# Performance work log

Hardware: AMD Instinct MI355X
Metric: run time of the kernel (lower is better)

The kernel has to match this reference:

```python
import jax, jax.numpy as jnp
from jax import lax
import numpy as np

B, T, F_IN = 64, 3072, 128
CONV_OUT, K, STRIDE = 64, 3, 3
HID, OUT = 256, 10


def setup_inputs() -> dict:
    key = jax.random.key(0)
    ks = jax.random.split(key, 10)
    s = 0.05
    return {
        "input": jax.random.normal(ks[0], (B, T, F_IN), jnp.float32),
        "r": jnp.zeros(((T - K) // STRIDE + 1, B, CONV_OUT), jnp.float32),
        "hx0": jax.random.normal(ks[1], (B, HID), jnp.float32),
        "cx0": jax.random.normal(ks[2], (B, HID), jnp.float32),
        "conv_w": jax.random.normal(ks[3], (CONV_OUT, F_IN, K), jnp.float32) * s,
        "conv_b": jnp.zeros((CONV_OUT,), jnp.float32),
        "w_ih": jax.random.normal(ks[4], (4 * HID, CONV_OUT), jnp.float32) * s,
        "b_ih": jnp.zeros((4 * HID,), jnp.float32),
        "w_hh": jax.random.normal(ks[5], (4 * HID, HID), jnp.float32) * s,
        "b_hh": jnp.zeros((4 * HID,), jnp.float32),
        "lin_w": jax.random.normal(ks[6], (OUT, HID), jnp.float32) * s,
        "lin_b": jnp.zeros((OUT,), jnp.float32),
        "batch_size": B,
    }


def reference(input, r, hx0, cx0, conv_w, conv_b, w_ih, b_ih, w_hh, b_hh, lin_w, lin_b, batch_size):
    # F.normalize: L2 normalize along dim=1 (the time dim), eps=1e-12
    norm = jnp.sqrt(jnp.sum(input * input, axis=1, keepdims=True))
    x = input / jnp.maximum(norm, 1e-12)
    x = jnp.transpose(x, (0, 2, 1))  # [B, F_IN, T]
    x = lax.conv_general_dilated(
        x, conv_w, window_strides=(STRIDE,), padding='VALID',
        dimension_numbers=('NCH', 'OIH', 'NCH')) + conv_b[None, :, None]
    x = jax.nn.relu(x)
    x = jnp.transpose(x, (2, 0, 1))  # [T', B, 64]

    def step(carry, xt):
        h, c = carry
        gates = xt @ w_ih.T + b_ih + h @ w_hh.T + b_hh  # [B, 4H]
        i, f, g, o = jnp.split(gates, 4, axis=-1)
        c = jax.nn.sigmoid(f) * c + jax.nn.sigmoid(i) * jnp.tanh(g)
        h = jax.nn.sigmoid(o) * jnp.tanh(c)
        return (h, c), None

    (h, _), _ = lax.scan(step, (hx0, cx0), x)
    return h @ lin_w.T + lin_b  # [B, OUT]
```

## Files before the change

kernel.cpp:

```cpp
#include <hip/hip_runtime.h>
#include <math.h>

#define B_N 64
#define T_N 3072
#define FIN 128
#define TP 1024
#define COUT 64
#define HID 256
#define G4 1024
#define OUT_N 10
#define NCHUNK 24
#define CHUNK_T (T_N / NCHUNK)

#define WREG 24
#define WLDS 8

typedef _Float16 h2_t __attribute__((ext_vector_type(2)));
typedef unsigned u32x4 __attribute__((ext_vector_type(4)));

#if defined(__has_builtin)
#if __has_builtin(__builtin_amdgcn_fdot2)
#define HAVE_FDOT2 1
#endif
#endif

__device__ __forceinline__ float fdot2(unsigned w, unsigned h, float acc) {
#ifdef HAVE_FDOT2
    return __builtin_amdgcn_fdot2(__builtin_bit_cast(h2_t, w),
                                  __builtin_bit_cast(h2_t, h), acc, false);
#else
    h2_t wv = __builtin_bit_cast(h2_t, w), hv = __builtin_bit_cast(h2_t, h);
    return acc + (float)wv.x * (float)hv.x + (float)wv.y * (float)hv.y;
#endif
}

__device__ __forceinline__ unsigned pack2(float a, float b) {
    unsigned la = (unsigned)__builtin_bit_cast(unsigned short, (_Float16)a);
    unsigned lb = (unsigned)__builtin_bit_cast(unsigned short, (_Float16)b);
    return la | (lb << 16);
}

__global__ void pack_weights(const float* __restrict__ w_ih,
                             const float* __restrict__ w_hh,
                             unsigned* __restrict__ whhR,
                             unsigned* __restrict__ whhL,
                             float* __restrict__ wihT) {
    int col = blockIdx.x, d = threadIdx.x;
    const float* wr = w_hh + col * HID;
    unsigned p = pack2(wr[2 * d], wr[2 * d + 1]);
    int c = d >> 2, r = d & 3;
    if (c < WREG) whhR[(c * 1024 + col) * 4 + r] = p;
    else          whhL[((c - WREG) * 1024 + col) * 4 + r] = p;
    if (d < COUT) wihT[d * 1024 + col] = w_ih[col * COUT + d];
}

__global__ void prep_conv_w(const float* __restrict__ conv_w, float* __restrict__ wc2) {
    int i = blockIdx.x * 256 + threadIdx.x;
    if (i < 24576) {
        int j = i >> 6, oc = i & 63;
        int kk = j >> 7, ic = j & 127;
        wc2[i] = conv_w[(oc * 128 + ic) * 3 + kk];
    }
}

__global__ void norm_partial(const float* __restrict__ in, float* __restrict__ part) {
    int b = blockIdx.x, ch = blockIdx.y, f = threadIdx.x;
    const float* p = in + ((size_t)b * T_N + (size_t)ch * CHUNK_T) * FIN + f;
    float s0 = 0.f, s1 = 0.f, s2 = 0.f, s3 = 0.f;
#pragma unroll
    for (int r = 0; r < CHUNK_T; r += 4) {
        float v0 = p[(r + 0) * FIN];
        float v1 = p[(r + 1) * FIN];
        float v2 = p[(r + 2) * FIN];
        float v3 = p[(r + 3) * FIN];
        s0 += v0 * v0; s1 += v1 * v1; s2 += v2 * v2; s3 += v3 * v3;
    }
    part[(b * NCHUNK + ch) * FIN + f] = (s0 + s1) + (s2 + s3);
}

__global__ __launch_bounds__(256) void conv_relu(
        const float* __restrict__ in, const float* __restrict__ part,
        const float* __restrict__ wc2, const float* __restrict__ cb,
        float* __restrict__ X) {
    __shared__ __align__(16) float xs[16 * 384];
    __shared__ __align__(16) float wsh[96 * 64];
    __shared__ float invn[FIN];

    int b = blockIdx.x, tile = blockIdx.y;
    int tid = threadIdx.x;

    if (tid < FIN) {
        float s = 0.f;
#pragma unroll
        for (int c = 0; c < NCHUNK; c++) s += part[(b * NCHUNK + c) * FIN + tid];
        invn[tid] = rsqrtf(fmaxf(s, 1e-24f));
    }
    __syncthreads();

    const float* ip = in + ((size_t)b * T_N + (size_t)tile * 48) * FIN;
    for (int i = tid; i < 6144; i += 256) xs[i] = ip[i] * invn[i & 127];

    int oc = tid & 63, tq = tid >> 6;
    float acc0 = 0.f, acc1 = 0.f, acc2 = 0.f, acc3 = 0.f;
    const float* xb = xs + tq * 4 * 384;

    for (int c = 0; c < 4; c++) {
        __syncthreads();
        for (int i = tid; i < 6144; i += 256) wsh[i] = wc2[c * 6144 + i];
        __syncthreads();
#pragma unroll 8
        for (int jj = 0; jj < 96; jj += 4) {
            int j = c * 96 + jj;
            float w0 = wsh[(jj + 0) * 64 + oc];
            float w1 = wsh[(jj + 1) * 64 + oc];
            float w2 = wsh[(jj + 2) * 64 + oc];
            float w3 = wsh[(jj + 3) * 64 + oc];
            float4 x0 = *(const float4*)(xb + j);
            float4 x1 = *(const float4*)(xb + 384 + j);
            float4 x2 = *(const float4*)(xb + 768 + j);
            float4 x3 = *(const float4*)(xb + 1152 + j);
            acc0 += w0 * x0.x + w1 * x0.y + w2 * x0.z + w3 * x0.w;
            acc1 += w0 * x1.x + w1 * x1.y + w2 * x1.z + w3 * x1.w;
            acc2 += w0 * x2.x + w1 * x2.y + w2 * x2.z + w3 * x2.w;
            acc3 += w0 * x3.x + w1 * x3.y + w2 * x3.z + w3 * x3.w;
        }
    }
    float bb = cb[oc];
    int tp0 = tile * 16 + tq * 4;
    size_t o = ((size_t)b * TP + tp0) * COUT + oc;
    X[o]       = fmaxf(acc0 + bb, 0.f);
    X[o + 64]  = fmaxf(acc1 + bb, 0.f);
    X[o + 128] = fmaxf(acc2 + bb, 0.f);
    X[o + 192] = fmaxf(acc3 + bb, 0.f);
}

__global__ __launch_bounds__(256) void x_gemm(
        const float* __restrict__ X, const float* __restrict__ wihT,
        const float* __restrict__ b_ih, const float* __restrict__ b_hh,
        _Float16* __restrict__ xg) {
    __shared__ float xs[64 * 17];
    int b = blockIdx.x, t0 = blockIdx.y * 16, tid = threadIdx.x;

    const float* Xp = X + ((size_t)b * TP + t0) * COUT;
    for (int i = tid; i < 1024; i += 256) {
        int r = i >> 6, k = i & 63;
        xs[k * 17 + r] = Xp[i];
    }
    __syncthreads();

#pragma unroll
    for (int jt = 0; jt < 4; jt++) {
        int jj = jt * 256 + tid;
        float bias = b_ih[jj] + b_hh[jj];
        float acc[16];
#pragma unroll
        for (int r = 0; r < 16; r++) acc[r] = bias;
        for (int k = 0; k < 64; k++) {
            float w = wihT[k * 1024 + jj];
#pragma unroll
            for (int r = 0; r < 16; r++) acc[r] += w * xs[k * 17 + r];
        }
#pragma unroll
        for (int r = 0; r < 16; r++)
            xg[((size_t)b * TP + t0 + r) * 1024 + jj] = (_Float16)acc[r];
    }
}

__device__ __forceinline__ float fsig(float x) {
    return 1.f / (1.f + __expf(-x));
}
__device__ __forceinline__ float ftanh(float x) {
    float xc = fminf(fmaxf(x, -15.f), 15.f);
    float e = __expf(2.f * xc);
    return (e - 1.f) / (e + 1.f);
}

#define SM_WL   0
#define SM_H    131072
#define SM_FO   131584
#define SM_H32  133632
#define SM_SIZE 134656

#define REP24(M) M(0) M(1) M(2) M(3) M(4) M(5) M(6) M(7) M(8) M(9) M(10) M(11) \
                 M(12) M(13) M(14) M(15) M(16) M(17) M(18) M(19) M(20) M(21) M(22) M(23)
#define REP8(M)  M(0) M(1) M(2) M(3) M(4) M(5) M(6) M(7)

#define DECLW(n)  u32x4 wa##n, wb##n;
#define LOADW(n)  wa##n = whhR4[(n) * 1024 + j]; wb##n = whhR4[(n) * 1024 + j + 512];
#define DOTCH(n)  { u32x4 H = hs4[n]; \
    a0 = fdot2(wa##n[0], H[0], a0); a1 = fdot2(wb##n[0], H[0], a1); \
    a0 = fdot2(wa##n[1], H[1], a0); a1 = fdot2(wb##n[1], H[1], a1); \
    a0 = fdot2(wa##n[2], H[2], a0); a1 = fdot2(wb##n[2], H[2], a1); \
    a0 = fdot2(wa##n[3], H[3], a0); a1 = fdot2(wb##n[3], H[3], a1); }
#define DOTLDS(m) { u32x4 WA = wL[(m) * 1024 + j]; u32x4 WB = wL[(m) * 1024 + j + 512]; \
    u32x4 H = hs4[WREG + (m)]; \
    a0 = fdot2(WA[0], H[0], a0); a1 = fdot2(WB[0], H[0], a1); \
    a0 = fdot2(WA[1], H[1], a0); a1 = fdot2(WB[1], H[1], a1); \
    a0 = fdot2(WA[2], H[2], a0); a1 = fdot2(WB[2], H[2], a1); \
    a0 = fdot2(WA[3], H[3], a0); a1 = fdot2(WB[3], H[3], a1); }

__global__ __attribute__((amdgpu_flat_work_group_size(512, 512),
                          amdgpu_waves_per_eu(2, 2)))
void lstm_kernel(
        const u32x4* __restrict__ whhR4, const u32x4* __restrict__ whhL4,
        const _Float16* __restrict__ xg,
        const float* __restrict__ hx0, const float* __restrict__ cx0,
        const float* __restrict__ lin_w, const float* __restrict__ lin_b,
        float* __restrict__ out) {
    extern __shared__ char smem[];
    u32x4*    wL    = (u32x4*)(smem + SM_WL);
    _Float16* h_s   = (_Float16*)(smem + SM_H);
    float2*   fo_s  = (float2*)(smem + SM_FO);
    float*    h32_s = (float*)(smem + SM_H32);

    const int b = blockIdx.x, j = threadIdx.x;

    REP24(DECLW)
    REP24(LOADW)

    for (int i = j; i < WLDS * 1024; i += 512) wL[i] = whhL4[i];

    float c_reg = 0.f;
    if (j < HID) {
        c_reg = cx0[b * HID + j];
        h_s[j] = (_Float16)hx0[b * HID + j];
    }
    const _Float16* Xg = xg + (size_t)b * TP * G4;
    _Float16 xa = Xg[j], xb = Xg[j + 512];
    __syncthreads();

    const u32x4* hs4 = (const u32x4*)h_s;

    for (int t = 0; t < TP; t++) {
        _Float16 xan = (_Float16)0.f, xbn = (_Float16)0.f;
        if (t + 1 < TP) {
            xan = Xg[(t + 1) * G4 + j];
            xbn = Xg[(t + 1) * G4 + j + 512];
        }

        float a0 = (float)xa, a1 = (float)xb;
        REP24(DOTCH)
        REP8(DOTLDS)

        float s0 = 0.f, s1 = 0.f;
        if (j >= HID) {
            fo_s[j - HID] = make_float2(fsig(a0), fsig(a1));
        } else {
            s0 = fsig(a0);
            s1 = ftanh(a1);
        }
        __syncthreads();
        if (j < HID) {
            float2 fo = fo_s[j];
            c_reg = fo.x * c_reg + s0 * s1;
            float hh = fo.y * ftanh(c_reg);
            h_s[j] = (_Float16)hh;
            if (t == TP - 1) h32_s[j] = hh;
        }
        __syncthreads();
        xa = xan; xb = xbn;
    }

    if (j < OUT_N) {
        float s = lin_b[j];
        const float* lw = lin_w + j * HID;
#pragma unroll 4
        for (int k = 0; k < HID; k++) s += h32_s[k] * lw[k];
        out[b * OUT_N + j] = s;
    }
}

extern "C" void kernel_launch(void* const* d_in, const int* in_sizes, int n_in,
                              void* d_out, int out_size, void* d_ws, size_t ws_size,
                              hipStream_t stream) {
    const float* input  = (const float*)d_in[0];
    const float* hx0    = (const float*)d_in[2];
    const float* cx0    = (const float*)d_in[3];
    const float* conv_w = (const float*)d_in[4];
    const float* conv_b = (const float*)d_in[5];
    const float* w_ih   = (const float*)d_in[6];
    const float* b_ih   = (const float*)d_in[7];
    const float* w_hh   = (const float*)d_in[8];
    const float* b_hh   = (const float*)d_in[9];
    const float* lin_w  = (const float*)d_in[10];
    const float* lin_b  = (const float*)d_in[11];

    float* ws = (float*)d_ws;
    float*     part = ws;
    float*     X    = part + 196608;
    float*     wc2  = X + 4194304;
    float*     wihT = wc2 + 24576;
    unsigned*  whhR = (unsigned*)(wihT + 65536);
    unsigned*  whhL = whhR + WREG * 1024 * 4;
    _Float16*  xg   = (_Float16*)(whhL + WLDS * 1024 * 4);

    (void)hipFuncSetAttribute((const void*)lstm_kernel,
                              hipFuncAttributeMaxDynamicSharedMemorySize, SM_SIZE);

    pack_weights<<<1024, 128, 0, stream>>>(w_ih, w_hh, whhR, whhL, wihT);
    prep_conv_w<<<96, 256, 0, stream>>>(conv_w, wc2);
    norm_partial<<<dim3(B_N, NCHUNK), FIN, 0, stream>>>(input, part);
    conv_relu<<<dim3(B_N, 64), 256, 0, stream>>>(input, part, wc2, conv_b, X);
    x_gemm<<<dim3(B_N, 64), 256, 0, stream>>>(X, wihT, b_ih, b_hh, xg);
    lstm_kernel<<<B_N, 512, SM_SIZE, stream>>>(
        (const u32x4*)whhR, (const u32x4*)whhL, xg,
        hx0, cx0, lin_w, lin_b, (float*)d_out);
}
```

Before: 2.539 ms.

## Interleave LSTM gate columns to drop one barrier per step and broadcast h via readlane

Gate columns are permuted so each thread pair holds (i,g) and (f,o) for the same hidden unit. The cell update is then finished inside the pair with a DPP lane swap, which removes the fo_s LDS exchange and one __syncthreads per timestep. h is double-buffered in LDS, loaded once per wave as a uint2 per lane and broadcast with readlane instead of vector LDS reads. x_gemm now writes the matching interleaved fp16 pairs. The readlane calls add SALU work, and the column interleave must stay consistent across both packing kernels.

```diff
diff --git a/kernel.cpp b/kernel.cpp
--- a/kernel.cpp
+++ b/kernel.cpp
@@ -40,17 +40,39 @@
     return la | (lb << 16);
 }
 
+__device__ __forceinline__ int gperm(int c) {
+    int sub = (c >> 9) & 1;
+    int cc  = c & 511;
+    int slot = (cc < 256) ? (cc << 1) : (((cc - 256) << 1) | 1);
+    return slot | (sub << 9);
+}
+
+__device__ __forceinline__ float swap1(float x) {
+    int i = __builtin_bit_cast(int, x);
+#if defined(__has_builtin)
+#if __has_builtin(__builtin_amdgcn_mov_dpp)
+    int r = __builtin_amdgcn_mov_dpp(i, 0xB1, 0xF, 0xF, true);
+#else
+    int r = __shfl_xor(i, 1, 64);
+#endif
+#else
+    int r = __shfl_xor(i, 1, 64);
+#endif
+    return __builtin_bit_cast(float, r);
+}
+
 __global__ void pack_weights(const float* __restrict__ w_ih,
                              const float* __restrict__ w_hh,
                              unsigned* __restrict__ whhR,
                              unsigned* __restrict__ whhL,
                              float* __restrict__ wihT) {
     int col = blockIdx.x, d = threadIdx.x;
+    int pcol = gperm(col);
     const float* wr = w_hh + col * HID;
     unsigned p = pack2(wr[2 * d], wr[2 * d + 1]);
     int c = d >> 2, r = d & 3;
-    if (c < WREG) whhR[(c * 1024 + col) * 4 + r] = p;
-    else          whhL[((c - WREG) * 1024 + col) * 4 + r] = p;
+    if (c < WREG) whhR[(c * 1024 + pcol) * 4 + r] = p;
+    else          whhL[((c - WREG) * 1024 + pcol) * 4 + r] = p;
     if (d < COUT) wihT[d * 1024 + col] = w_ih[col * COUT + d];
 }
 
@@ -148,21 +170,30 @@
     }
     __syncthreads();
 
-#pragma unroll
-    for (int jt = 0; jt < 4; jt++) {
-        int jj = jt * 256 + tid;
-        float bias = b_ih[jj] + b_hh[jj];
-        float acc[16];
-#pragma unroll
-        for (int r = 0; r < 16; r++) acc[r] = bias;
+    unsigned* xgu = (unsigned*)xg;
+#pragma unroll
+    for (int half = 0; half < 2; half++) {
+        int cA = half * 512 + tid;
+        int cB = cA + 256;
+        float bA = b_ih[cA] + b_hh[cA];
+        float bB = b_ih[cB] + b_hh[cB];
+        float accA[16], accB[16];
+#pragma unroll
+        for (int r = 0; r < 16; r++) { accA[r] = bA; accB[r] = bB; }
         for (int k = 0; k < 64; k++) {
-            float w = wihT[k * 1024 + jj];
-#pragma unroll
-            for (int r = 0; r < 16; r++) acc[r] += w * xs[k * 17 + r];
+            float wA = wihT[k * 1024 + cA];
+            float wB = wihT[k * 1024 + cB];
+#pragma unroll
+            for (int r = 0; r < 16; r++) {
+                float xv = xs[k * 17 + r];
+                accA[r] += wA * xv;
+                accB[r] += wB * xv;
+            }
         }
 #pragma unroll
         for (int r = 0; r < 16; r++)
-            xg[((size_t)b * TP + t0 + r) * 1024 + jj] = (_Float16)acc[r];
+            xgu[((size_t)b * TP + t0 + r) * 512 + half * 256 + tid] =
+                pack2(accA[r], accB[r]);
     }
 }
 
@@ -177,9 +208,8 @@
 
 #define SM_WL   0
 #define SM_H    131072
-#define SM_FO   131584
-#define SM_H32  133632
-#define SM_SIZE 134656
+#define SM_H32  132096
+#define SM_SIZE 133120
 
 #define REP24(M) M(0) M(1) M(2) M(3) M(4) M(5) M(6) M(7) M(8) M(9) M(10) M(11) \
                  M(12) M(13) M(14) M(15) M(16) M(17) M(18) M(19) M(20) M(21) M(22) M(23)
@@ -187,17 +217,26 @@
 
 #define DECLW(n)  u32x4 wa##n, wb##n;
 #define LOADW(n)  wa##n = whhR4[(n) * 1024 + j]; wb##n = whhR4[(n) * 1024 + j + 512];
-#define DOTCH(n)  { u32x4 H = hs4[n]; \
-    a0 = fdot2(wa##n[0], H[0], a0); a1 = fdot2(wb##n[0], H[0], a1); \
-    a0 = fdot2(wa##n[1], H[1], a0); a1 = fdot2(wb##n[1], H[1], a1); \
-    a0 = fdot2(wa##n[2], H[2], a0); a1 = fdot2(wb##n[2], H[2], a1); \
-    a0 = fdot2(wa##n[3], H[3], a0); a1 = fdot2(wb##n[3], H[3], a1); }
+
+#define DOTCH(n)  { \
+    unsigned h0 = (unsigned)__builtin_amdgcn_readlane((int)hvv.x, 2 * (n)); \
+    unsigned h1 = (unsigned)__builtin_amdgcn_readlane((int)hvv.y, 2 * (n)); \
+    unsigned h2 = (unsigned)__builtin_amdgcn_readlane((int)hvv.x, 2 * (n) + 1); \
+    unsigned h3 = (unsigned)__builtin_amdgcn_readlane((int)hvv.y, 2 * (n) + 1); \
+    a0 = fdot2(wa##n[0], h0, a0); a1 = fdot2(wb##n[0], h0, a1); \
+    a0 = fdot2(wa##n[1], h1, a0); a1 = fdot2(wb##n[1], h1, a1); \
+    a0 = fdot2(wa##n[2], h2, a0); a1 = fdot2(wb##n[2], h2, a1); \
+    a0 = fdot2(wa##n[3], h3, a0); a1 = fdot2(wb##n[3], h3, a1); }
+
 #define DOTLDS(m) { u32x4 WA = wL[(m) * 1024 + j]; u32x4 WB = wL[(m) * 1024 + j + 512]; \
-    u32x4 H = hs4[WREG + (m)]; \
-    a0 = fdot2(WA[0], H[0], a0); a1 = fdot2(WB[0], H[0], a1); \
-    a0 = fdot2(WA[1], H[1], a0); a1 = fdot2(WB[1], H[1], a1); \
-    a0 = fdot2(WA[2], H[2], a0); a1 = fdot2(WB[2], H[2], a1); \
-    a0 = fdot2(WA[3], H[3], a0); a1 = fdot2(WB[3], H[3], a1); }
+    unsigned h0 = (unsigned)__builtin_amdgcn_readlane((int)hvv.x, 2 * (WREG + (m))); \
+    unsigned h1 = (unsigned)__builtin_amdgcn_readlane((int)hvv.y, 2 * (WREG + (m))); \
+    unsigned h2 = (unsigned)__builtin_amdgcn_readlane((int)hvv.x, 2 * (WREG + (m)) + 1); \
+    unsigned h3 = (unsigned)__builtin_amdgcn_readlane((int)hvv.y, 2 * (WREG + (m)) + 1); \
+    a0 = fdot2(WA[0], h0, a0); a1 = fdot2(WB[0], h0, a1); \
+    a0 = fdot2(WA[1], h1, a0); a1 = fdot2(WB[1], h1, a1); \
+    a0 = fdot2(WA[2], h2, a0); a1 = fdot2(WB[2], h2, a1); \
+    a0 = fdot2(WA[3], h3, a0); a1 = fdot2(WB[3], h3, a1); }
 
 __global__ __attribute__((amdgpu_flat_work_group_size(512, 512),
                           amdgpu_waves_per_eu(2, 2)))
@@ -209,11 +248,13 @@
         float* __restrict__ out) {
     extern __shared__ char smem[];
     u32x4*    wL    = (u32x4*)(smem + SM_WL);
-    _Float16* h_s   = (_Float16*)(smem + SM_H);
-    float2*   fo_s  = (float2*)(smem + SM_FO);
+    _Float16* hbuf  = (_Float16*)(smem + SM_H);
     float*    h32_s = (float*)(smem + SM_H32);
 
     const int b = blockIdx.x, j = threadIdx.x;
+    const int lane = j & 63;
+    const int m = j >> 1;
+    const int odd = j & 1;
 
     REP24(DECLW)
     REP24(LOADW)
@@ -221,17 +262,17 @@
     for (int i = j; i < WLDS * 1024; i += 512) wL[i] = whhL4[i];
 
     float c_reg = 0.f;
-    if (j < HID) {
-        c_reg = cx0[b * HID + j];
-        h_s[j] = (_Float16)hx0[b * HID + j];
-    }
+    if (odd) c_reg = cx0[b * HID + m];
+    if (j < HID) hbuf[j] = (_Float16)hx0[b * HID + j];
+
     const _Float16* Xg = xg + (size_t)b * TP * G4;
     _Float16 xa = Xg[j], xb = Xg[j + 512];
     __syncthreads();
 
-    const u32x4* hs4 = (const u32x4*)h_s;
-
     for (int t = 0; t < TP; t++) {
+        const uint2* hp = (const uint2*)(hbuf + (t & 1) * 256);
+        uint2 hvv = hp[lane];
+
         _Float16 xan = (_Float16)0.f, xbn = (_Float16)0.f;
         if (t + 1 < TP) {
             xan = Xg[(t + 1) * G4 + j];
@@ -242,20 +283,15 @@
         REP24(DOTCH)
         REP8(DOTLDS)
 
-        float s0 = 0.f, s1 = 0.f;
-        if (j >= HID) {
-            fo_s[j - HID] = make_float2(fsig(a0), fsig(a1));
-        } else {
-            s0 = fsig(a0);
-            s1 = ftanh(a1);
-        }
-        __syncthreads();
-        if (j < HID) {
-            float2 fo = fo_s[j];
-            c_reg = fo.x * c_reg + s0 * s1;
-            float hh = fo.y * ftanh(c_reg);
-            h_s[j] = (_Float16)hh;
-            if (t == TP - 1) h32_s[j] = hh;
+        float sa = fsig(a0);
+        float p  = sa * ftanh(a1);
+        float pn = swap1(p);
+        if (odd) {
+            float so = fsig(a1);
+            c_reg = sa * c_reg + pn;
+            float hh = so * ftanh(c_reg);
+            hbuf[((t + 1) & 1) * 256 + m] = (_Float16)hh;
+            if (t == TP - 1) h32_s[m] = hh;
         }
         __syncthreads();
         xa = xan; xb = xbn;
```

New measurement: 2.594 ms. +2.2%, slower.

## Stream a third of recurrent weights from L2 each step instead of registers

Applied to the files above, without the earlier changes.

Splits the w_hh fp16 weights into three parts: 12 chunks kept in registers, 12 chunks reloaded from global memory (L2) every timestep, and 8 chunks in LDS. The streamed loads are issued in two halves, each interleaved with other dot-product work so their latency can overlap. Empty asm barriers pin the register-resident weights and stop the compiler from hoisting the streamed loads out of the time loop. The aim is to cut register pressure and spilling from holding 24 chunks, at the cost of repeated global/L2 traffic on the serial recurrent critical path.

```diff
diff --git a/kernel.cpp b/kernel.cpp
--- a/kernel.cpp
+++ b/kernel.cpp
@@ -12,7 +12,8 @@
 #define NCHUNK 24
 #define CHUNK_T (T_N / NCHUNK)
 
-#define WREG 24
+#define WREG 12
+#define WSTR 12
 #define WLDS 8
 
 typedef _Float16 h2_t __attribute__((ext_vector_type(2)));
@@ -43,14 +44,16 @@
 __global__ void pack_weights(const float* __restrict__ w_ih,
                              const float* __restrict__ w_hh,
                              unsigned* __restrict__ whhR,
+                             unsigned* __restrict__ whhS,
                              unsigned* __restrict__ whhL,
                              float* __restrict__ wihT) {
     int col = blockIdx.x, d = threadIdx.x;
     const float* wr = w_hh + col * HID;
     unsigned p = pack2(wr[2 * d], wr[2 * d + 1]);
     int c = d >> 2, r = d & 3;
-    if (c < WREG) whhR[(c * 1024 + col) * 4 + r] = p;
-    else          whhL[((c - WREG) * 1024 + col) * 4 + r] = p;
+    if (c < WREG)             whhR[(c * 1024 + col) * 4 + r] = p;
+    else if (c < WREG + WSTR) whhS[((c - WREG) * 1024 + col) * 4 + r] = p;
+    else                      whhL[((c - WREG - WSTR) * 1024 + col) * 4 + r] = p;
     if (d < COUT) wihT[d * 1024 + col] = w_ih[col * COUT + d];
 }
 
@@ -181,19 +184,28 @@
 #define SM_H32  133632
 #define SM_SIZE 134656
 
-#define REP24(M) M(0) M(1) M(2) M(3) M(4) M(5) M(6) M(7) M(8) M(9) M(10) M(11) \
-                 M(12) M(13) M(14) M(15) M(16) M(17) M(18) M(19) M(20) M(21) M(22) M(23)
+#define REP12(M) M(0) M(1) M(2) M(3) M(4) M(5) M(6) M(7) M(8) M(9) M(10) M(11)
 #define REP8(M)  M(0) M(1) M(2) M(3) M(4) M(5) M(6) M(7)
 
 #define DECLW(n)  u32x4 wa##n, wb##n;
 #define LOADW(n)  wa##n = whhR4[(n) * 1024 + j]; wb##n = whhR4[(n) * 1024 + j + 512];
+
 #define DOTCH(n)  { u32x4 H = hs4[n]; \
     a0 = fdot2(wa##n[0], H[0], a0); a1 = fdot2(wb##n[0], H[0], a1); \
     a0 = fdot2(wa##n[1], H[1], a0); a1 = fdot2(wb##n[1], H[1], a1); \
     a0 = fdot2(wa##n[2], H[2], a0); a1 = fdot2(wb##n[2], H[2], a1); \
     a0 = fdot2(wa##n[3], H[3], a0); a1 = fdot2(wb##n[3], H[3], a1); }
+
+#define SDECL(q)  u32x4 sa##q, sb##q;
+#define SLOADQ(q) sa##q = sp[(q) * 1024 + j]; sb##q = sp[(q) * 1024 + j + 512];
+#define DOTSTR(q) { u32x4 H = hs4[WREG + (q)]; \
+    a0 = fdot2(sa##q[0], H[0], a0); a1 = fdot2(sb##q[0], H[0], a1); \
+    a0 = fdot2(sa##q[1], H[1], a0); a1 = fdot2(sb##q[1], H[1], a1); \
+    a0 = fdot2(sa##q[2], H[2], a0); a1 = fdot2(sb##q[2], H[2], a1); \
+    a0 = fdot2(sa##q[3], H[3], a0); a1 = fdot2(sb##q[3], H[3], a1); }
+
 #define DOTLDS(m) { u32x4 WA = wL[(m) * 1024 + j]; u32x4 WB = wL[(m) * 1024 + j + 512]; \
-    u32x4 H = hs4[WREG + (m)]; \
+    u32x4 H = hs4[WREG + WSTR + (m)]; \
     a0 = fdot2(WA[0], H[0], a0); a1 = fdot2(WB[0], H[0], a1); \
     a0 = fdot2(WA[1], H[1], a0); a1 = fdot2(WB[1], H[1], a1); \
     a0 = fdot2(WA[2], H[2], a0); a1 = fdot2(WB[2], H[2], a1); \
@@ -202,7 +214,8 @@
 __global__ __attribute__((amdgpu_flat_work_group_size(512, 512),
                           amdgpu_waves_per_eu(2, 2)))
 void lstm_kernel(
-        const u32x4* __restrict__ whhR4, const u32x4* __restrict__ whhL4,
+        const u32x4* __restrict__ whhR4, const u32x4* __restrict__ whhS4,
+        const u32x4* __restrict__ whhL4,
         const _Float16* __restrict__ xg,
         const float* __restrict__ hx0, const float* __restrict__ cx0,
         const float* __restrict__ lin_w, const float* __restrict__ lin_b,
@@ -215,8 +228,15 @@
 
     const int b = blockIdx.x, j = threadIdx.x;
 
-    REP24(DECLW)
-    REP24(LOADW)
+    REP12(DECLW)
+    REP12(LOADW)
+    asm volatile("" :
+        "+v"(wa0), "+v"(wb0), "+v"(wa1), "+v"(wb1),
+        "+v"(wa2), "+v"(wb2), "+v"(wa3), "+v"(wb3),
+        "+v"(wa4), "+v"(wb4), "+v"(wa5), "+v"(wb5),
+        "+v"(wa6), "+v"(wb6), "+v"(wa7), "+v"(wb7),
+        "+v"(wa8), "+v"(wb8), "+v"(wa9), "+v"(wb9),
+        "+v"(wa10), "+v"(wb10), "+v"(wa11), "+v"(wb11));
 
     for (int i = j; i < WLDS * 1024; i += 512) wL[i] = whhL4[i];
 
@@ -232,6 +252,13 @@
     const u32x4* hs4 = (const u32x4*)h_s;
 
     for (int t = 0; t < TP; t++) {
+        const u32x4* sp = whhS4;
+        asm volatile("" : "+v"(sp));
+
+        SDECL(0) SDECL(1) SDECL(2) SDECL(3) SDECL(4) SDECL(5)
+        SDECL(6) SDECL(7) SDECL(8) SDECL(9) SDECL(10) SDECL(11)
+        SLOADQ(0) SLOADQ(1) SLOADQ(2) SLOADQ(3) SLOADQ(4) SLOADQ(5)
+
         _Float16 xan = (_Float16)0.f, xbn = (_Float16)0.f;
         if (t + 1 < TP) {
             xan = Xg[(t + 1) * G4 + j];
@@ -239,8 +266,15 @@
         }
 
         float a0 = (float)xa, a1 = (float)xb;
-        REP24(DOTCH)
-        REP8(DOTLDS)
+        DOTCH(0) DOTCH(1) DOTCH(2) DOTCH(3) DOTCH(4) DOTCH(5)
+        DOTCH(6) DOTCH(7) DOTCH(8) DOTCH(9) DOTCH(10) DOTCH(11)
+
+        SLOADQ(6) SLOADQ(7) SLOADQ(8) SLOADQ(9) SLOADQ(10) SLOADQ(11)
+
+        DOTSTR(0) DOTSTR(1) DOTSTR(2) DOTSTR(3) DOTSTR(4) DOTSTR(5)
+        DOTLDS(0) DOTLDS(1) DOTLDS(2) DOTLDS(3)
+        DOTLDS(4) DOTLDS(5) DOTLDS(6) DOTLDS(7)
+        DOTSTR(6) DOTSTR(7) DOTSTR(8) DOTSTR(9) DOTSTR(10) DOTSTR(11)
 
         float s0 = 0.f, s1 = 0.f;
         if (j >= HID) {
@@ -291,18 +325,19 @@
     float*     wc2  = X + 4194304;
     float*     wihT = wc2 + 24576;
     unsigned*  whhR = (unsigned*)(wihT + 65536);
-    unsigned*  whhL = whhR + WREG * 1024 * 4;
+    unsigned*  whhS = whhR + WREG * 1024 * 4;
+    unsigned*  whhL = whhS + WSTR * 1024 * 4;
     _Float16*  xg   = (_Float16*)(whhL + WLDS * 1024 * 4);
 
     (void)hipFuncSetAttribute((const void*)lstm_kernel,
                               hipFuncAttributeMaxDynamicSharedMemorySize, SM_SIZE);
 
-    pack_weights<<<1024, 128, 0, stream>>>(w_ih, w_hh, whhR, whhL, wihT);
+    pack_weights<<<1024, 128, 0, stream>>>(w_ih, w_hh, whhR, whhS, whhL, wihT);
     prep_conv_w<<<96, 256, 0, stream>>>(conv_w, wc2);
     norm_partial<<<dim3(B_N, NCHUNK), FIN, 0, stream>>>(input, part);
     conv_relu<<<dim3(B_N, 64), 256, 0, stream>>>(input, part, wc2, conv_b, X);
     x_gemm<<<dim3(B_N, 64), 256, 0, stream>>>(X, wihT, b_ih, b_hh, xg);
     lstm_kernel<<<B_N, 512, SM_SIZE, stream>>>(
-        (const u32x4*)whhR, (const u32x4*)whhL, xg,
+        (const u32x4*)whhR, (const u32x4*)whhS, (const u32x4*)whhL, xg,
         hx0, cx0, lin_w, lin_b, (float*)d_out);
 }
```

New measurement: 3.326 ms. +31.0%, slower.
